# Optimization experiments

Measured on AMD Instinct MI355X. Metric: run time of the kernel, lower is better.

## Reference

```python
import jax, jax.numpy as jnp
import numpy as np

D_MODEL = 1024
N_HEADS = 16
MAX_LAG = 512
D_K = D_MODEL // N_HEADS


def setup_inputs() -> dict:
    key = jax.random.key(0)
    ks = jax.random.split(key, 11)
    B, S = 2, 2048
    x = jax.random.normal(ks[0], (B, S, D_MODEL), dtype=jnp.float32)
    lag = jax.random.randint(ks[1], (S,), 0, MAX_LAG + 1, dtype=jnp.int64)
    scale = 1.0 / np.sqrt(D_MODEL)
    wq = jax.random.normal(ks[2], (D_MODEL, D_MODEL), dtype=jnp.float32) * scale
    bq = jnp.zeros((D_MODEL,), dtype=jnp.float32)
    wk = jax.random.normal(ks[3], (D_MODEL, D_MODEL), dtype=jnp.float32) * scale
    bk = jnp.zeros((D_MODEL,), dtype=jnp.float32)
    wv = jax.random.normal(ks[4], (D_MODEL, D_MODEL), dtype=jnp.float32) * scale
    bv = jnp.zeros((D_MODEL,), dtype=jnp.float32)
    wo = jax.random.normal(ks[5], (D_MODEL, D_MODEL), dtype=jnp.float32) * scale
    bo = jnp.zeros((D_MODEL,), dtype=jnp.float32)
    lag_bias = jax.random.normal(ks[6], (N_HEADS, MAX_LAG + 1), dtype=jnp.float32) * 0.02
    return {"x": x, "lag": lag, "wq": wq, "bq": bq, "wk": wk, "bk": bk,
            "wv": wv, "bv": bv, "wo": wo, "bo": bo, "lag_bias": lag_bias}


def reference(x, lag, wq, bq, wk, bk, wv, bv, wo, bo, lag_bias):
    B, S, D = x.shape
    H, dk = N_HEADS, D_K
    # projections: torch Linear is x @ W.T + b; here weights stored as (in, out)
    q = (x @ wq + bq).reshape(B, S, H, dk).transpose(0, 2, 1, 3)  # (B,H,S,dk)
    k = (x @ wk + bk).reshape(B, S, H, dk).transpose(0, 2, 1, 3)
    v = (x @ wv + bv).reshape(B, S, H, dk).transpose(0, 2, 1, 3)
    scores = jnp.einsum('bhqd,bhkd->bhqk', q, k) / jnp.sqrt(jnp.float32(dk))
    ld = jnp.abs(lag[:, None] - lag[None, :]).astype(jnp.int32)  # (S,S)
    bias = lag_bias[:, ld]  # (H,S,S)
    attn = jax.nn.softmax(scores + bias[None], axis=-1)
    out = jnp.einsum('bhqk,bhkd->bhqd', attn, v)
    out = out.transpose(0, 2, 1, 3).reshape(B, S, D)
    return out @ wo + bo
```

## Files before the change

kernel.cpp:

```cpp
#include <hip/hip_runtime.h>

typedef __bf16 bf16;
typedef __bf16 bf16x8 __attribute__((ext_vector_type(8)));
typedef float f32x4 __attribute__((ext_vector_type(4)));

__device__ __forceinline__ f32x4 mfma16(bf16x8 a, bf16x8 b, f32x4 c) {
  return __builtin_amdgcn_mfma_f32_16x16x32_bf16(a, b, c, 0, 0, 0);
}
__device__ __forceinline__ void gload16(const bf16* g, bf16* l) {
  __builtin_amdgcn_global_load_lds((const __attribute__((address_space(1))) unsigned int*)g,
                                   (__attribute__((address_space(3))) unsigned int*)l, 16, 0, 0);
}

__global__ __launch_bounds__(256) void cvt_x_kernel(const float* __restrict__ in,
                                                    bf16* __restrict__ out, int n8) {
  int i = blockIdx.x * 256 + threadIdx.x;
  if (i >= n8) return;
  const float4* p = (const float4*)in + (size_t)i * 2;
  float4 f0 = p[0], f1 = p[1];
  bf16x8 o;
  o[0] = (bf16)f0.x; o[1] = (bf16)f0.y; o[2] = (bf16)f0.z; o[3] = (bf16)f0.w;
  o[4] = (bf16)f1.x; o[5] = (bf16)f1.y; o[6] = (bf16)f1.z; o[7] = (bf16)f1.w;
  *((bf16x8*)out + i) = o;
}

__global__ __launch_bounds__(256) void cvt_wt_kernel(const float* __restrict__ in,
                                                     bf16* __restrict__ out) {
  __shared__ float t[64][68];
  int bx = blockIdx.x & 15;
  int by = blockIdx.x >> 4;
  int tid = threadIdx.x;
  int r = tid >> 2, p = tid & 3;
  const float* src = in + (size_t)(by * 64 + r) * 1024 + bx * 64 + p * 16;
#pragma unroll
  for (int j = 0; j < 16; j += 4)
    *(float4*)&t[r][p * 16 + j] = *(const float4*)(src + j);
  __syncthreads();
  int n = tid >> 2, sp = tid & 3;
  bf16 tmp[16];
#pragma unroll
  for (int j = 0; j < 16; ++j) tmp[j] = (bf16)t[sp * 16 + j][n];
  bf16* dst = out + (size_t)(bx * 64 + n) * 1024 + by * 64 + sp * 16;
  *(bf16x8*)dst = *(bf16x8*)&tmp[0];
  *(bf16x8*)(dst + 8) = *(bf16x8*)&tmp[8];
}

__global__ void cvt_bias_kernel(const float* __restrict__ bq, const float* __restrict__ bk,
                                const float* __restrict__ bv, float* __restrict__ out) {
  int i = blockIdx.x * 256 + threadIdx.x;
  if (i < 1024) out[i] = bq[i];
  else if (i < 2048) out[i] = bk[i - 1024];
  else if (i < 3072) out[i] = bv[i - 2048];
}

template <int OUT_BF16>
__global__ __launch_bounds__(256) void gemm_bt_kernel(
    const bf16* __restrict__ A, const bf16* __restrict__ Bt,
    const float* __restrict__ bias, void* __restrict__ C,
    int M, int N, int K, int scale_cols, float scale_val) {
  __shared__ bf16 As[128][40];
  __shared__ bf16 Bs[128][40];
  int bn = blockIdx.x * 128, bm = blockIdx.y * 128;
  int tid = threadIdx.x;
  int l = tid & 63;
  int w = tid >> 6;
  int wr = w >> 1, wc = w & 1;
  int g = l >> 4, c = l & 15;
  int sr = tid >> 2, sk = (tid & 3) * 8;
  const bf16* Ap = A + (size_t)(bm + sr) * K + sk;
  const bf16* Bp = Bt + (size_t)(bn + sr) * K + sk;
  f32x4 acc[4][4] = {};
  for (int k0 = 0; k0 < K; k0 += 32) {
    bf16x8 a0 = *(const bf16x8*)(Ap + k0);
    bf16x8 a1 = *(const bf16x8*)(Ap + (size_t)64 * K + k0);
    bf16x8 b0 = *(const bf16x8*)(Bp + k0);
    bf16x8 b1 = *(const bf16x8*)(Bp + (size_t)64 * K + k0);
    __syncthreads();
    *(bf16x8*)&As[sr][sk] = a0;
    *(bf16x8*)&As[sr + 64][sk] = a1;
    *(bf16x8*)&Bs[sr][sk] = b0;
    *(bf16x8*)&Bs[sr + 64][sk] = b1;
    __syncthreads();
    bf16x8 af[4], bfr[4];
#pragma unroll
    for (int m = 0; m < 4; ++m) af[m] = *(const bf16x8*)&As[wr * 64 + m * 16 + c][g * 8];
#pragma unroll
    for (int n = 0; n < 4; ++n) bfr[n] = *(const bf16x8*)&Bs[wc * 64 + n * 16 + c][g * 8];
#pragma unroll
    for (int m = 0; m < 4; ++m)
#pragma unroll
      for (int n = 0; n < 4; ++n)
        acc[m][n] = mfma16(af[m], bfr[n], acc[m][n]);
  }
  int rowb = bm + wr * 64;
  int colb = bn + wc * 64;
#pragma unroll
  for (int n = 0; n < 4; ++n) {
    int col = colb + n * 16 + c;
    float bv = bias[col];
    float s = (col < scale_cols) ? scale_val : 1.0f;
#pragma unroll
    for (int m = 0; m < 4; ++m) {
      int row = rowb + m * 16 + g * 4;
#pragma unroll
      for (int j = 0; j < 4; ++j) {
        float v = (acc[m][n][j] + bv) * s;
        if (OUT_BF16)
          ((bf16*)C)[(size_t)(row + j) * N + col] = (bf16)v;
        else
          ((float*)C)[(size_t)(row + j) * N + col] = v;
      }
    }
  }
}

__global__ __launch_bounds__(256) void transpose_v_kernel(const bf16* __restrict__ qkv,
                                                          bf16* __restrict__ vt) {
  __shared__ bf16 t[64][72];
  int blk = blockIdx.x;
  int st = blk & 31;
  int h = (blk >> 5) & 15;
  int b = blk >> 9;
  int tid = threadIdx.x;
  int r = tid >> 2, p = tid & 3;
  const bf16* src = qkv + (size_t)(b * 2048 + st * 64 + r) * 3072 + 2048 + h * 64 + p * 16;
  *(bf16x8*)&t[r][p * 16] = *(const bf16x8*)src;
  *(bf16x8*)&t[r][p * 16 + 8] = *(const bf16x8*)(src + 8);
  __syncthreads();
  int d = tid >> 2, sp = tid & 3;
  bf16 tmp[16];
#pragma unroll
  for (int j = 0; j < 16; ++j) tmp[j] = t[sp * 16 + j][d];
  bf16* dst = vt + (size_t)((b * 16 + h) * 64 + d) * 2048 + st * 64 + sp * 16;
  *(bf16x8*)dst = *(bf16x8*)&tmp[0];
  *(bf16x8*)(dst + 8) = *(bf16x8*)&tmp[8];
}

__global__ __launch_bounds__(256) void attn_kernel(
    const bf16* __restrict__ qkv, const bf16* __restrict__ vt,
    const int* __restrict__ lag, const float* __restrict__ lag_bias,
    bf16* __restrict__ out) {
  __shared__ __align__(16) bf16 Ks0[64 * 64];
  __shared__ __align__(16) bf16 Vs0[64 * 64];
  __shared__ __align__(16) bf16 Ks1[64 * 64];
  __shared__ __align__(16) bf16 Vs1[64 * 64];
  __shared__ __align__(16) bf16 Ps[4][32][72];
  __shared__ float bias_s[516];
  __shared__ int lag_s[2048];

  int blk = blockIdx.x;
  blk = (blk & 7) * 64 + (blk >> 3);
  int qt = blk & 15;
  int h = (blk >> 4) & 15;
  int b = blk >> 8;
  int tid = threadIdx.x;
  int w = tid >> 6, l = tid & 63, g = l >> 4, c = l & 15;

  for (int i = tid; i < 513; i += 256) bias_s[i] = lag_bias[h * 513 + i] * 1.44269504f;
  for (int i = tid; i < 2048; i += 256) lag_s[i] = lag[i];

  int q0 = qt * 128 + w * 32;
  const bf16* qbase = qkv + (size_t)(b * 2048 + q0) * 3072 + h * 64;
  bf16x8 qf[2][2];
#pragma unroll
  for (int m = 0; m < 2; ++m)
#pragma unroll
    for (int kh = 0; kh < 2; ++kh)
      qf[m][kh] = *(const bf16x8*)(qbase + (size_t)(m * 16 + c) * 3072 + kh * 32 + g * 8);

  int swz = (c & 7) << 3;
  int off0 = (g * 8) ^ swz;
  int off1 = off0 ^ 32;

  int r0 = w * 16 + (l >> 3);
  int colE = ((l & 7) ^ (l >> 3)) << 3;
  const bf16* kbase = qkv + (size_t)(b * 2048) * 3072 + 1024 + h * 64;
  const bf16* vbase = vt + (size_t)(b * 16 + h) * 64 * 2048;
  const bf16* kg0 = kbase + (size_t)r0 * 3072 + colE;
  const bf16* kg1 = kbase + (size_t)(r0 + 8) * 3072 + colE;
  const bf16* vg0 = vbase + (size_t)r0 * 2048 + colE;
  const bf16* vg1 = vbase + (size_t)(r0 + 8) * 2048 + colE;

#define STAGE(KD, VD)                    \
  do {                                   \
    gload16(kg0, KD + w * 1024);         \
    gload16(kg1, KD + w * 1024 + 512);   \
    gload16(vg0, VD + w * 1024);         \
    gload16(vg1, VD + w * 1024 + 512);   \
    kg0 += 64 * 3072; kg1 += 64 * 3072;  \
    vg0 += 64; vg1 += 64;                \
  } while (0)

  STAGE(Ks0, Vs0);
  __syncthreads();

  int lagq[2][4];
#pragma unroll
  for (int m = 0; m < 2; ++m)
#pragma unroll
    for (int j = 0; j < 4; ++j) lagq[m][j] = lag_s[q0 + m * 16 + g * 4 + j];

  f32x4 oacc[2][4] = {};
  float psum[2][4] = {};

#define TILE(KB, VB, KT)                                                          \
  do {                                                                            \
    f32x4 sf[2][4] = {};                                                          \
    int lagk[4];                                                                  \
    _Pragma("unroll") for (int kb = 0; kb < 4; ++kb) {                            \
      int row = kb * 16 + c;                                                      \
      bf16x8 k0 = *(const bf16x8*)&KB[row * 64 + off0];                           \
      bf16x8 k1 = *(const bf16x8*)&KB[row * 64 + off1];                           \
      sf[0][kb] = mfma16(qf[0][0], k0, sf[0][kb]);                                \
      sf[0][kb] = mfma16(qf[0][1], k1, sf[0][kb]);                                \
      sf[1][kb] = mfma16(qf[1][0], k0, sf[1][kb]);                                \
      sf[1][kb] = mfma16(qf[1][1], k1, sf[1][kb]);                                \
      lagk[kb] = lag_s[(KT) + kb * 16 + c];                                       \
    }                                                                             \
    _Pragma("unroll") for (int m = 0; m < 2; ++m)                                 \
    _Pragma("unroll") for (int kb = 0; kb < 4; ++kb)                              \
    _Pragma("unroll") for (int j = 0; j < 4; ++j) {                               \
      int ld = lagq[m][j] - lagk[kb];                                             \
      ld = ld < 0 ? -ld : ld;                                                     \
      float p = __builtin_amdgcn_exp2f(sf[m][kb][j] + bias_s[ld]);                \
      psum[m][j] += p;                                                            \
      Ps[w][m * 16 + g * 4 + j][kb * 16 + c] = (bf16)p;                           \
    }                                                                             \
    asm volatile("s_waitcnt lgkmcnt(0)" ::: "memory");                            \
    _Pragma("unroll") for (int ph = 0; ph < 2; ++ph) {                            \
      bf16x8 pa0 = *(const bf16x8*)&Ps[w][c][ph * 32 + g * 8];                    \
      bf16x8 pa1 = *(const bf16x8*)&Ps[w][16 + c][ph * 32 + g * 8];               \
      int voff = ph ? off1 : off0;                                                \
      _Pragma("unroll") for (int n = 0; n < 4; ++n) {                             \
        bf16x8 vf = *(const bf16x8*)&VB[(n * 16 + c) * 64 + voff];                \
        oacc[0][n] = mfma16(pa0, vf, oacc[0][n]);                                 \
        oacc[1][n] = mfma16(pa1, vf, oacc[1][n]);                                 \
      }                                                                           \
    }                                                                             \
  } while (0)

  for (int kt = 0; kt < 2048; kt += 128) {
    if (kt + 64 < 2048) STAGE(Ks1, Vs1);
    TILE(Ks0, Vs0, kt);
    __syncthreads();
    if (kt + 128 < 2048) STAGE(Ks0, Vs0);
    TILE(Ks1, Vs1, kt + 64);
    __syncthreads();
  }

#pragma unroll
  for (int m = 0; m < 2; ++m) {
#pragma unroll
    for (int j = 0; j < 4; ++j) {
      float s = psum[m][j];
      s += __shfl_xor(s, 1);
      s += __shfl_xor(s, 2);
      s += __shfl_xor(s, 4);
      s += __shfl_xor(s, 8);
      float inv = 1.f / s;
      bf16* ob = out + (size_t)(b * 2048 + q0 + m * 16 + g * 4 + j) * 1024 + h * 64;
#pragma unroll
      for (int n = 0; n < 4; ++n)
        ob[n * 16 + c] = (bf16)(oacc[m][n][j] * inv);
    }
  }
#undef STAGE
#undef TILE
}

extern "C" void kernel_launch(void* const* d_in, const int* in_sizes, int n_in,
                              void* d_out, int out_size, void* d_ws, size_t ws_size,
                              hipStream_t stream) {
  const float* x        = (const float*)d_in[0];
  const int*   lag      = (const int*)d_in[1];
  const float* wq       = (const float*)d_in[2];
  const float* bq       = (const float*)d_in[3];
  const float* wk       = (const float*)d_in[4];
  const float* bk       = (const float*)d_in[5];
  const float* wv       = (const float*)d_in[6];
  const float* bv       = (const float*)d_in[7];
  const float* wo       = (const float*)d_in[8];
  const float* bo       = (const float*)d_in[9];
  const float* lag_bias = (const float*)d_in[10];

  char* ws = (char*)d_ws;
  bf16*  xb    = (bf16*)ws;
  bf16*  wqkvt = (bf16*)(ws + (8u  << 20));
  bf16*  wot   = (bf16*)(ws + (14u << 20));
  float* bqkv  = (float*)(ws + (16u << 20));
  bf16*  qkv   = (bf16*)(ws + (17u << 20));
  bf16*  vtb   = (bf16*)(ws + (41u << 20));
  bf16*  aout  = (bf16*)(ws + (49u << 20));

  cvt_x_kernel<<<2048, 256, 0, stream>>>(x, xb, 524288);
  cvt_wt_kernel<<<256, 256, 0, stream>>>(wq, wqkvt);
  cvt_wt_kernel<<<256, 256, 0, stream>>>(wk, wqkvt + (1u << 20));
  cvt_wt_kernel<<<256, 256, 0, stream>>>(wv, wqkvt + (2u << 20));
  cvt_wt_kernel<<<256, 256, 0, stream>>>(wo, wot);
  cvt_bias_kernel<<<12, 256, 0, stream>>>(bq, bk, bv, bqkv);
  gemm_bt_kernel<1><<<dim3(24, 32), 256, 0, stream>>>(
      xb, wqkvt, bqkv, qkv, 4096, 3072, 1024, 1024, 0.125f * 1.44269504f);
  transpose_v_kernel<<<1024, 256, 0, stream>>>(qkv, vtb);
  attn_kernel<<<512, 256, 0, stream>>>(qkv, vtb, lag, lag_bias, aout);
  gemm_bt_kernel<0><<<dim3(8, 32), 256, 0, stream>>>(
      aout, wot, bo, (float*)d_out, 4096, 1024, 1024, 0, 1.0f);
}
```

Measured before the change: 171.0 us.

## Use direct global-to-LDS loads with XOR swizzle in GEMM, add MFMA priority hints

The projection GEMM now stages tiles with global_load_lds straight into shared memory instead of going through registers. It uses a 64-wide K step and an XOR-swizzled LDS layout so fragment reads avoid bank conflicts. This halves the number of barrier pairs per K and drops the register round trip. The attention kernel also wraps its MFMA sections in s_setprio so those waves get issue priority over the softmax and exp work of other waves. Still single-buffered, so load latency is not overlapped with compute.

```diff
diff --git a/kernel.cpp b/kernel.cpp
--- a/kernel.cpp
+++ b/kernel.cpp
@@ -58,39 +58,47 @@
     const bf16* __restrict__ A, const bf16* __restrict__ Bt,
     const float* __restrict__ bias, void* __restrict__ C,
     int M, int N, int K, int scale_cols, float scale_val) {
-  __shared__ bf16 As[128][40];
-  __shared__ bf16 Bs[128][40];
+  __shared__ __align__(16) bf16 As[128 * 64];
+  __shared__ __align__(16) bf16 Bs[128 * 64];
   int bn = blockIdx.x * 128, bm = blockIdx.y * 128;
   int tid = threadIdx.x;
   int l = tid & 63;
   int w = tid >> 6;
   int wr = w >> 1, wc = w & 1;
   int g = l >> 4, c = l & 15;
-  int sr = tid >> 2, sk = (tid & 3) * 8;
-  const bf16* Ap = A + (size_t)(bm + sr) * K + sk;
-  const bf16* Bp = Bt + (size_t)(bn + sr) * K + sk;
+  int swz = (c & 7) << 3;
+
+  int srow = l >> 3;
+  int scol = ((l & 7) ^ srow) << 3;
+  const bf16* Ap = A + (size_t)(bm + w * 32 + srow) * K + scol;
+  const bf16* Bp = Bt + (size_t)(bn + w * 32 + srow) * K + scol;
+  bf16* AsW = As + w * 32 * 64;
+  bf16* BsW = Bs + w * 32 * 64;
+
   f32x4 acc[4][4] = {};
-  for (int k0 = 0; k0 < K; k0 += 32) {
-    bf16x8 a0 = *(const bf16x8*)(Ap + k0);
-    bf16x8 a1 = *(const bf16x8*)(Ap + (size_t)64 * K + k0);
-    bf16x8 b0 = *(const bf16x8*)(Bp + k0);
-    bf16x8 b1 = *(const bf16x8*)(Bp + (size_t)64 * K + k0);
+  for (int k0 = 0; k0 < K; k0 += 64) {
     __syncthreads();
-    *(bf16x8*)&As[sr][sk] = a0;
-    *(bf16x8*)&As[sr + 64][sk] = a1;
-    *(bf16x8*)&Bs[sr][sk] = b0;
-    *(bf16x8*)&Bs[sr + 64][sk] = b1;
+#pragma unroll
+    for (int i = 0; i < 4; ++i) {
+      gload16(Ap + (size_t)(8 * i) * K + k0, AsW + i * 512);
+      gload16(Bp + (size_t)(8 * i) * K + k0, BsW + i * 512);
+    }
     __syncthreads();
-    bf16x8 af[4], bfr[4];
-#pragma unroll
-    for (int m = 0; m < 4; ++m) af[m] = *(const bf16x8*)&As[wr * 64 + m * 16 + c][g * 8];
-#pragma unroll
-    for (int n = 0; n < 4; ++n) bfr[n] = *(const bf16x8*)&Bs[wc * 64 + n * 16 + c][g * 8];
-#pragma unroll
-    for (int m = 0; m < 4; ++m)
+#pragma unroll
+    for (int kh = 0; kh < 2; ++kh) {
+      bf16x8 af[4], bfr[4];
+#pragma unroll
+      for (int m = 0; m < 4; ++m)
+        af[m] = *(const bf16x8*)&As[(wr * 64 + m * 16 + c) * 64 + ((kh * 32 + g * 8) ^ swz)];
 #pragma unroll
       for (int n = 0; n < 4; ++n)
-        acc[m][n] = mfma16(af[m], bfr[n], acc[m][n]);
+        bfr[n] = *(const bf16x8*)&Bs[(wc * 64 + n * 16 + c) * 64 + ((kh * 32 + g * 8) ^ swz)];
+#pragma unroll
+      for (int m = 0; m < 4; ++m)
+#pragma unroll
+        for (int n = 0; n < 4; ++n)
+          acc[m][n] = mfma16(af[m], bfr[n], acc[m][n]);
+    }
   }
   int rowb = bm + wr * 64;
   int colb = bn + wc * 64;
@@ -207,6 +215,7 @@
   do {                                                                            \
     f32x4 sf[2][4] = {};                                                          \
     int lagk[4];                                                                  \
+    __builtin_amdgcn_s_setprio(1);                                                \
     _Pragma("unroll") for (int kb = 0; kb < 4; ++kb) {                            \
       int row = kb * 16 + c;                                                      \
       bf16x8 k0 = *(const bf16x8*)&KB[row * 64 + off0];                           \
@@ -217,6 +226,7 @@
       sf[1][kb] = mfma16(qf[1][1], k1, sf[1][kb]);                                \
       lagk[kb] = lag_s[(KT) + kb * 16 + c];                                       \
     }                                                                             \
+    __builtin_amdgcn_s_setprio(0);                                                \
     _Pragma("unroll") for (int m = 0; m < 2; ++m)                                 \
     _Pragma("unroll") for (int kb = 0; kb < 4; ++kb)                              \
     _Pragma("unroll") for (int j = 0; j < 4; ++j) {                               \
@@ -227,6 +237,7 @@
       Ps[w][m * 16 + g * 4 + j][kb * 16 + c] = (bf16)p;                           \
     }                                                                             \
     asm volatile("s_waitcnt lgkmcnt(0)" ::: "memory");                            \
+    __builtin_amdgcn_s_setprio(1);                                                \
     _Pragma("unroll") for (int ph = 0; ph < 2; ++ph) {                            \
       bf16x8 pa0 = *(const bf16x8*)&Ps[w][c][ph * 32 + g * 8];                    \
       bf16x8 pa1 = *(const bf16x8*)&Ps[w][16 + c][ph * 32 + g * 8];               \
@@ -237,6 +248,7 @@
         oacc[1][n] = mfma16(pa1, vf, oacc[1][n]);                                 \
       }                                                                           \
     }                                                                             \
+    __builtin_amdgcn_s_setprio(0);                                                \
   } while (0)
 
   for (int kt = 0; kt < 2048; kt += 128) {
```

Measured after the change: 170.8 us. About the same (-0.1%).
